# Kernel tuning notes

Hardware: AMD Instinct MI355X
Metric: run time of the kernel (lower is better)

The kernel has to match this reference:

```python
import jax, jax.numpy as jnp
import numpy as np

N, E, F_IN, HID, EF, C = 100000, 1600000, 64, 64, 32, 4

def setup_inputs() -> dict:
    key = jax.random.key(0)
    ks = jax.random.split(key, 24)
    def p(k, shape, scale=0.05):
        return jax.random.normal(k, shape, dtype=jnp.float32) * scale
    return dict(
        x=jax.random.normal(ks[0], (N, F_IN), dtype=jnp.float32),
        edge_index=jax.random.randint(ks[1], (2, E), 0, N, dtype=jnp.int32),
        edge_attr=jax.random.normal(ks[2], (E, EF), dtype=jnp.float32),
        # GCNConv weights for update (z), reset (r), candidate (h) gates
        Wz=p(ks[3], (F_IN, HID)), bz=jnp.zeros((HID,), jnp.float32),
        Wr=p(ks[4], (F_IN, HID)), br=jnp.zeros((HID,), jnp.float32),
        Wh=p(ks[5], (F_IN, HID)), bh=jnp.zeros((HID,), jnp.float32),
        # gate linear layers: Linear(2*HID, HID)
        Wlz=p(ks[6], (2 * HID, HID)), blz=jnp.zeros((HID,), jnp.float32),
        Wlr=p(ks[7], (2 * HID, HID)), blr=jnp.zeros((HID,), jnp.float32),
        Wlh=p(ks[8], (2 * HID, HID)), blh=jnp.zeros((HID,), jnp.float32),
        # edge predictor MLP: Linear(2*HID+EF, HID) -> ReLU -> Dropout(eval) -> Linear(HID, C)
        W1=p(ks[9], (2 * HID + EF, HID)), b1=jnp.zeros((HID,), jnp.float32),
        W2=p(ks[10], (HID, C)), b2=jnp.zeros((C,), jnp.float32),
    )

def _gcn(x, W, b, src, dst, norm, n):
    # GCNConv: out = D^-1/2 (A+I) D^-1/2 (x @ W) + b; src/dst already include self-loops
    xw = x @ W  # [N, HID]
    agg = jax.ops.segment_sum(xw[src] * norm[:, None], dst, num_segments=n)
    return agg + b

def reference(x, edge_index, edge_attr, Wz, bz, Wr, br, Wh, bh,
              Wlz, blz, Wlr, blr, Wlh, blh, W1, b1, W2, b2):
    n = x.shape[0]
    src, dst = edge_index[0], edge_index[1]
    # add self-loops for GCN normalization
    loop = jnp.arange(n, dtype=src.dtype)
    s = jnp.concatenate([src, loop])
    d = jnp.concatenate([dst, loop])
    deg = jax.ops.segment_sum(jnp.ones(s.shape[0], dtype=x.dtype), d, num_segments=n)
    dinv = jax.lax.rsqrt(jnp.maximum(deg, 1.0))
    norm = dinv[s] * dinv[d]  # symmetric normalization per edge
    # TGCN cell, initial hidden state H = zeros
    H0 = jnp.zeros((n, Wz.shape[1]), dtype=x.dtype)
    Z = jax.nn.sigmoid(jnp.concatenate([_gcn(x, Wz, bz, s, d, norm, n), H0], axis=1) @ Wlz + blz)
    R = jax.nn.sigmoid(jnp.concatenate([_gcn(x, Wr, br, s, d, norm, n), H0], axis=1) @ Wlr + blr)
    Ht = jnp.tanh(jnp.concatenate([_gcn(x, Wh, bh, s, d, norm, n), H0 * R], axis=1) @ Wlh + blh)
    h = Z * H0 + (1.0 - Z) * Ht  # [N, HID]
    # edge predictor on original edges (no self-loops)
    emb = jnp.concatenate([h[src], h[dst], edge_attr], axis=1)  # [E, 2*HID+EF]
    hid = jax.nn.relu(emb @ W1 + b1)  # Dropout(0.5) is identity in eval mode
    return hid @ W2 + b2  # [E, C]
```

## Files before the change

kernel.cpp:

```cpp
#include <hip/hip_runtime.h>

#define F 64
#define EF 32
#define COUT 4

typedef unsigned int uint;
typedef unsigned short ushort;
typedef __attribute__((ext_vector_type(8))) short bf16x8;
typedef __attribute__((ext_vector_type(4))) float f32x4;

__device__ inline ushort f2bf(float f) {
    uint u = __float_as_uint(f);
    return (ushort)((u + 0x7fff + ((u >> 16) & 1)) >> 16);
}
__device__ inline float bf2f(ushort u) {
    return __uint_as_float(((uint)u) << 16);
}


__global__ void k_deg(const int* __restrict__ dst, int* __restrict__ deg, int E) {
    int i = blockIdx.x * blockDim.x + threadIdx.x;
    if (i < E) atomicAdd(&deg[dst[i]], 1);
}

__global__ void k_dinv(const int* __restrict__ deg, float* __restrict__ dinv, int n) {
    int i = blockIdx.x * blockDim.x + threadIdx.x;
    if (i < n) dinv[i] = rsqrtf((float)(deg[i] + 1));
}

__global__ void k_xcast(const float* __restrict__ x, ushort* __restrict__ xb, int n4) {
    int i = blockIdx.x * 256 + threadIdx.x;
    if (i >= n4) return;
    float4 v = *(const float4*)(x + (size_t)i * 4);
    ushort4 o;
    o.x = f2bf(v.x); o.y = f2bf(v.y); o.z = f2bf(v.z); o.w = f2bf(v.w);
    *(ushort4*)(xb + (size_t)i * 4) = o;
}


__global__ void k_blocksum(const int* __restrict__ deg, int* __restrict__ bsum, int n) {
    __shared__ int sm[256];
    int i = blockIdx.x * 256 + threadIdx.x;
    sm[threadIdx.x] = (i < n) ? deg[i] : 0;
    __syncthreads();
    for (int s = 128; s > 0; s >>= 1) {
        if (threadIdx.x < s) sm[threadIdx.x] += sm[threadIdx.x + s];
        __syncthreads();
    }
    if (threadIdx.x == 0) bsum[blockIdx.x] = sm[0];
}

__global__ void k_scanb(const int* __restrict__ bsum, int* __restrict__ boffs, int nb) {
    int lane = threadIdx.x;
    int carry = 0;
    for (int base = 0; base < nb; base += 64) {
        int v = (base + lane < nb) ? bsum[base + lane] : 0;
        int incl = v;
        #pragma unroll
        for (int off = 1; off < 64; off <<= 1) {
            int t = __shfl_up(incl, off);
            if (lane >= off) incl += t;
        }
        if (base + lane < nb) boffs[base + lane] = carry + incl - v;
        carry += __shfl(incl, 63);
    }
}

__global__ void k_rowptr(const int* __restrict__ deg, const int* __restrict__ boffs,
                         int* __restrict__ rowptr, int n) {
    __shared__ int sm[256];
    int tid = threadIdx.x;
    int i = blockIdx.x * 256 + tid;
    int v = (i < n) ? deg[i] : 0;
    sm[tid] = v;
    __syncthreads();
    for (int off = 1; off < 256; off <<= 1) {
        int t = (tid >= off) ? sm[tid - off] : 0;
        __syncthreads();
        sm[tid] += t;
        __syncthreads();
    }
    if (i < n) rowptr[i] = boffs[blockIdx.x] + sm[tid] - v;
}

__global__ void k_bucket(const int* __restrict__ src, const int* __restrict__ dst,
                         const int* __restrict__ rowptr, int* __restrict__ fill,
                         int2* __restrict__ es2, int E) {
    int e = blockIdx.x * 256 + threadIdx.x;
    if (e >= E) return;
    int d = dst[e];
    int pos = rowptr[d] + atomicAdd(&fill[d], 1);
    es2[pos] = make_int2(src[e], e);
}

__global__ void k_expand(const int* __restrict__ rowptr, const int* __restrict__ deg,
                         int* __restrict__ edst, int n) {
    int i = blockIdx.x * 256 + threadIdx.x;
    if (i >= n) return;
    int p = rowptr[i], c = deg[i];
    for (int j = 0; j < c; ++j) edst[p + j] = i;
}

__global__ __launch_bounds__(256) void k_agg(
    const ushort* __restrict__ xb, const float* __restrict__ dinv,
    const int2* __restrict__ es2, const int* __restrict__ rowptr,
    const int* __restrict__ deg, ushort* __restrict__ xaggb, int n) {
    int node = (blockIdx.x * 256 + threadIdx.x) >> 6;
    int lane = threadIdx.x & 63;
    if (node >= n) return;
    int start = rowptr[node], cnt = deg[node];
    float di = dinv[node];
    float acc = bf2f(xb[(size_t)node * F + lane]) * di * di;
    for (int base = 0; base < cnt; base += 64) {
        int m = min(64, cnt - base);
        int s = 0; float dv = 0.f;
        if (lane < m) { s = es2[start + base + lane].x; dv = dinv[s]; }
        for (int i = 0; i < m; ++i) {
            int si = __shfl(s, i);
            float wv = __shfl(dv, i) * di;
            acc += bf2f(xb[(size_t)si * F + lane]) * wv;
        }
    }
    xaggb[(size_t)node * F + lane] = f2bf(acc);
}

__global__ void k_weights(const float* __restrict__ Wz, const float* __restrict__ bz,
                          const float* __restrict__ Wh, const float* __restrict__ bh,
                          const float* __restrict__ Wlz, const float* __restrict__ blz,
                          const float* __restrict__ Wlh, const float* __restrict__ blh,
                          ushort* __restrict__ B1t, float* __restrict__ V) {
    int j = threadIdx.x;
    int k = blockIdx.x;
    if (k < 64) {
        float sz = 0.f, sh = 0.f;
        for (int i = 0; i < 64; ++i) {
            sz += Wz[k * 64 + i] * Wlz[i * 64 + j];
            sh += Wh[k * 64 + i] * Wlh[i * 64 + j];
        }
        B1t[j * 64 + k]        = f2bf(sz);
        B1t[(64 + j) * 64 + k] = f2bf(sh);
    } else {
        float sz = blz[j], sh = blh[j];
        for (int i = 0; i < 64; ++i) {
            sz += bz[i] * Wlz[i * 64 + j];
            sh += bh[i] * Wlh[i * 64 + j];
        }
        V[j]      = sz;
        V[64 + j] = sh;
    }
}

__global__ void k_wcast(const float* __restrict__ W1, ushort* __restrict__ B2t,
                        ushort* __restrict__ W1cTb) {
    int i = blockIdx.x * 256 + threadIdx.x;
    if (i < 8192) {
        int c = i >> 6, k = i & 63;
        int row = (c < 64) ? k : (64 + k);
        B2t[i] = f2bf(W1[row * 64 + (c & 63)]);
    }
    int t = i - 8192;
    if (t >= 0 && t < 2048) {
        int j = t >> 5, k = t & 31;
        W1cTb[t] = f2bf(W1[(128 + k) * 64 + j]);
    }
}

__global__ __launch_bounds__(256) void k_node(
    const ushort* __restrict__ xaggb, const ushort* __restrict__ B1t,
    const ushort* __restrict__ B2t, const float* __restrict__ V,
    const float* __restrict__ b1,
    ushort* __restrict__ Pb, ushort* __restrict__ Qb, int n) {
    __shared__ ushort hsm[64 * 64];
    int wid = threadIdx.x >> 6, lane = threadIdx.x & 63;
    int lg = lane >> 4, lc = lane & 15;
    int base = blockIdx.x * 64;

    bf16x8 b1f[2][2], b2f[2][2];
    #pragma unroll
    for (int t = 0; t < 2; ++t) {
        int c1 = ((t ? wid + 4 : wid) * 16 + lc) * 64;
        int c2 = ((wid * 2 + t) * 16 + lc) * 64;
        #pragma unroll
        for (int ks = 0; ks < 2; ++ks) {
            b1f[t][ks] = *(const bf16x8*)(B1t + c1 + ks * 32 + lg * 8);
            b2f[t][ks] = *(const bf16x8*)(B2t + c2 + ks * 32 + lg * 8);
        }
    }
    float vzc = V[wid * 16 + lc], vhc = V[64 + wid * 16 + lc];
    float bP[2];
    #pragma unroll
    for (int t = 0; t < 2; ++t) {
        int c2 = (wid * 2 + t) * 16 + lc;
        bP[t] = (c2 < 64) ? b1[c2] : 0.f;
    }

    const f32x4 fz = {0.f, 0.f, 0.f, 0.f};
    f32x4 accZ[4], accT[4];
    #pragma unroll
    for (int rt = 0; rt < 4; ++rt) { accZ[rt] = fz; accT[rt] = fz; }

    #pragma unroll
    for (int rt = 0; rt < 4; ++rt) {
        const ushort* ap = xaggb + (size_t)(base + rt * 16 + lc) * 64 + lg * 8;
        bf16x8 a0 = *(const bf16x8*)(ap);
        bf16x8 a1 = *(const bf16x8*)(ap + 32);
        accZ[rt] = __builtin_amdgcn_mfma_f32_16x16x32_bf16(a0, b1f[0][0], accZ[rt], 0, 0, 0);
        accZ[rt] = __builtin_amdgcn_mfma_f32_16x16x32_bf16(a1, b1f[0][1], accZ[rt], 0, 0, 0);
        accT[rt] = __builtin_amdgcn_mfma_f32_16x16x32_bf16(a0, b1f[1][0], accT[rt], 0, 0, 0);
        accT[rt] = __builtin_amdgcn_mfma_f32_16x16x32_bf16(a1, b1f[1][1], accT[rt], 0, 0, 0);
    }

    #pragma unroll
    for (int rt = 0; rt < 4; ++rt) {
        #pragma unroll
        for (int r = 0; r < 4; ++r) {
            float z = 1.f / (1.f + __expf(-(accZ[rt][r] + vzc)));
            float tt = tanhf(accT[rt][r] + vhc);
            float h = (1.f - z) * tt;
            int row = rt * 16 + lg * 4 + r;
            int byte = ((row * 64 + wid * 16 + lc) * 2) ^ ((row & 7) << 4);
            *(ushort*)((char*)hsm + byte) = f2bf(h);
        }
    }
    __syncthreads();

    f32x4 acc2[2][4];
    #pragma unroll
    for (int rt = 0; rt < 4; ++rt) { acc2[0][rt] = fz; acc2[1][rt] = fz; }
    #pragma unroll
    for (int rt = 0; rt < 4; ++rt) {
        #pragma unroll
        for (int ks = 0; ks < 2; ++ks) {
            int row = rt * 16 + lc;
            int byte = (row * 128 + ks * 64 + lg * 16) ^ ((row & 7) << 4);
            bf16x8 a2 = *(const bf16x8*)((char*)hsm + byte);
            acc2[0][rt] = __builtin_amdgcn_mfma_f32_16x16x32_bf16(a2, b2f[0][ks], acc2[0][rt], 0, 0, 0);
            acc2[1][rt] = __builtin_amdgcn_mfma_f32_16x16x32_bf16(a2, b2f[1][ks], acc2[1][rt], 0, 0, 0);
        }
    }

    ushort* dstb = (wid < 2) ? Pb : Qb;
    #pragma unroll
    for (int t = 0; t < 2; ++t) {
        int cl = ((wid * 2 + t) * 16 + lc) & 63;
        #pragma unroll
        for (int rt = 0; rt < 4; ++rt) {
            #pragma unroll
            for (int r = 0; r < 4; ++r) {
                int node = base + rt * 16 + lg * 4 + r;
                if (node < n) dstb[(size_t)node * 64 + cl] = f2bf(acc2[t][rt][r] + bP[t]);
            }
        }
    }
}

__global__ __launch_bounds__(256) void k_edge2(
    const int2* __restrict__ es2, const int* __restrict__ edst,
    const float* __restrict__ attr,
    const ushort* __restrict__ Pb, const ushort* __restrict__ Qb,
    const ushort* __restrict__ W1cTb,
    const float* __restrict__ W2, const float* __restrict__ b2,
    float* __restrict__ out, int E) {
    int wid = threadIdx.x >> 6, lane = threadIdx.x & 63;
    int lg = lane >> 4, lc = lane & 15;
    int we = (blockIdx.x * 4 + wid) * 64;
    if (we >= E) return;

    int idx = we + lane; if (idx >= E) idx = E - 1;
    int2 se = es2[idx];
    int sR = se.x, eidR = se.y, dR = edst[idx];

    bf16x8 aW[4];
    #pragma unroll
    for (int rt = 0; rt < 4; ++rt)
        aW[rt] = *(const bf16x8*)(W1cTb + (rt * 16 + lc) * 32 + lg * 8);

    float4 w2r[4][4];
    #pragma unroll
    for (int rt = 0; rt < 4; ++rt)
        #pragma unroll
        for (int r = 0; r < 4; ++r)
            w2r[rt][r] = *(const float4*)(W2 + (rt * 16 + lg * 4 + r) * 4);
    float4 b2v = *(const float4*)(b2);

    const f32x4 fz = {0.f, 0.f, 0.f, 0.f};
    #pragma unroll
    for (int et = 0; et < 4; ++et) {
        int erow = et * 16 + lc;
        int eid_e = __shfl(eidR, erow);
        int s_e   = __shfl(sR, erow);
        int d_e   = __shfl(dR, erow);

        const float* ap = attr + (size_t)eid_e * EF + lg * 8;
        float4 a0 = *(const float4*)(ap);
        float4 a1 = *(const float4*)(ap + 4);
        bf16x8 bfr;
        bfr[0] = (short)f2bf(a0.x); bfr[1] = (short)f2bf(a0.y);
        bfr[2] = (short)f2bf(a0.z); bfr[3] = (short)f2bf(a0.w);
        bfr[4] = (short)f2bf(a1.x); bfr[5] = (short)f2bf(a1.y);
        bfr[6] = (short)f2bf(a1.z); bfr[7] = (short)f2bf(a1.w);

        f32x4 acc[4];
        #pragma unroll
        for (int rt = 0; rt < 4; ++rt) acc[rt] = fz;
        #pragma unroll
        for (int rt = 0; rt < 4; ++rt)
            acc[rt] = __builtin_amdgcn_mfma_f32_16x16x32_bf16(aW[rt], bfr, acc[rt], 0, 0, 0);

        const ushort* Ps = Pb + (size_t)s_e * F;
        const ushort* Qd = Qb + (size_t)d_e * F;
        float o0 = 0.f, o1 = 0.f, o2 = 0.f, o3 = 0.f;
        #pragma unroll
        for (int rt = 0; rt < 4; ++rt) {
            int j0 = rt * 16 + lg * 4;
            uint2 pv = *(const uint2*)(Ps + j0);
            uint2 qv = *(const uint2*)(Qd + j0);
            float p0 = __uint_as_float(pv.x << 16), p1 = __uint_as_float(pv.x & 0xffff0000u);
            float p2 = __uint_as_float(pv.y << 16), p3 = __uint_as_float(pv.y & 0xffff0000u);
            float q0 = __uint_as_float(qv.x << 16), q1 = __uint_as_float(qv.x & 0xffff0000u);
            float q2 = __uint_as_float(qv.y << 16), q3 = __uint_as_float(qv.y & 0xffff0000u);
            float h0 = fmaxf(acc[rt][0] + p0 + q0, 0.f);
            float h1 = fmaxf(acc[rt][1] + p1 + q1, 0.f);
            float h2 = fmaxf(acc[rt][2] + p2 + q2, 0.f);
            float h3 = fmaxf(acc[rt][3] + p3 + q3, 0.f);
            o0 += h0 * w2r[rt][0].x + h1 * w2r[rt][1].x + h2 * w2r[rt][2].x + h3 * w2r[rt][3].x;
            o1 += h0 * w2r[rt][0].y + h1 * w2r[rt][1].y + h2 * w2r[rt][2].y + h3 * w2r[rt][3].y;
            o2 += h0 * w2r[rt][0].z + h1 * w2r[rt][1].z + h2 * w2r[rt][2].z + h3 * w2r[rt][3].z;
            o3 += h0 * w2r[rt][0].w + h1 * w2r[rt][1].w + h2 * w2r[rt][2].w + h3 * w2r[rt][3].w;
        }
        o0 += __shfl_xor(o0, 16); o0 += __shfl_xor(o0, 32);
        o1 += __shfl_xor(o1, 16); o1 += __shfl_xor(o1, 32);
        o2 += __shfl_xor(o2, 16); o2 += __shfl_xor(o2, 32);
        o3 += __shfl_xor(o3, 16); o3 += __shfl_xor(o3, 32);
        if (lg == 0 && (we + erow) < E)
            *(float4*)(out + (size_t)eid_e * 4) =
                make_float4(o0 + b2v.x, o1 + b2v.y, o2 + b2v.z, o3 + b2v.w);
    }
}


extern "C" void kernel_launch(void* const* d_in, const int* in_sizes, int n_in,
                              void* d_out, int out_size, void* d_ws, size_t ws_size,
                              hipStream_t stream) {
    const float* x    = (const float*)d_in[0];
    const int*   ei   = (const int*)d_in[1];
    const float* attr = (const float*)d_in[2];
    const float* Wz   = (const float*)d_in[3];
    const float* bz   = (const float*)d_in[4];
    const float* Wh   = (const float*)d_in[7];
    const float* bh   = (const float*)d_in[8];
    const float* Wlz  = (const float*)d_in[9];
    const float* blz  = (const float*)d_in[10];
    const float* Wlh  = (const float*)d_in[13];
    const float* blh  = (const float*)d_in[14];
    const float* W1   = (const float*)d_in[15];
    const float* b1   = (const float*)d_in[16];
    const float* W2   = (const float*)d_in[17];
    const float* b2   = (const float*)d_in[18];
    float* out = (float*)d_out;

    const int N = in_sizes[0] / F;
    const int E = in_sizes[1] / 2;
    const int* src = ei;
    const int* dst = ei + E;
    const int NB = (N + 255) / 256;
    const int NBT = (N + 63) / 64;

    ushort* xaggb = (ushort*)d_ws;
    ushort* regB  = xaggb + (size_t)N * F;
    ushort* Qb    = regB + (size_t)N * F;
    ushort* B1t   = Qb + (size_t)N * F;
    ushort* B2t   = B1t + 8192;
    ushort* W1cTb = B2t + 8192;
    float*  V     = (float*)(W1cTb + 2048);
    int2*   es2   = (int2*)(V + 128);
    int*    edst  = (int*)(es2 + (size_t)E);
    int*    deg   = edst + E;
    float*  dinv  = (float*)(deg + N);
    int*    rowptr= (int*)(dinv + N);
    int*    fill  = rowptr + N;
    int*    bsum  = fill + N;
    int*    boffs = bsum + 512;
    ushort* xb = regB;
    ushort* Pb = regB;

    hipMemsetAsync(deg, 0, (size_t)N * sizeof(int), stream);
    hipMemsetAsync(fill, 0, (size_t)N * sizeof(int), stream);

    k_deg<<<(E + 255) / 256, 256, 0, stream>>>(dst, deg, E);
    k_dinv<<<NB, 256, 0, stream>>>(deg, dinv, N);
    k_weights<<<65, 64, 0, stream>>>(Wz, bz, Wh, bh, Wlz, blz, Wlh, blh, B1t, V);
    k_wcast<<<40, 256, 0, stream>>>(W1, B2t, W1cTb);
    k_xcast<<<(N * F / 4 + 255) / 256, 256, 0, stream>>>(x, xb, N * F / 4);

    k_blocksum<<<NB, 256, 0, stream>>>(deg, bsum, N);
    k_scanb<<<1, 64, 0, stream>>>(bsum, boffs, NB);
    k_rowptr<<<NB, 256, 0, stream>>>(deg, boffs, rowptr, N);
    k_bucket<<<(E + 255) / 256, 256, 0, stream>>>(src, dst, rowptr, fill, es2, E);
    k_expand<<<NB, 256, 0, stream>>>(rowptr, deg, edst, N);

    k_agg<<<(N * 64 + 255) / 256, 256, 0, stream>>>(xb, dinv, es2, rowptr, deg, xaggb, N);

    k_node<<<NBT, 256, 0, stream>>>(xaggb, B1t, B2t, V, b1, Pb, Qb, N);

    k_edge2<<<(E + 255) / 256, 256, 0, stream>>>(es2, edst, attr, Pb, Qb, W1cTb, W2, b2, out, E);
}
```

Baseline: 430.2 us.

## Process four neighbors per wave in GCN aggregation and stage W2 in LDS

The aggregation kernel changes from one neighbor per iteration across 64 lanes to four neighbors at once. Each 16-lane group loads 4 bf16 features as a uint2 and the groups are combined with xor shuffles. This cuts the serial loop trip count per node by four and widens memory accesses, at the cost of idle lanes on the tail and an extra reduction. The edge kernel also loads W2 and b2 into shared memory instead of keeping 64 float4 registers per thread, which lowers register pressure to improve occupancy but adds a block sync and LDS reads.

```diff
diff --git a/kernel.cpp b/kernel.cpp
--- a/kernel.cpp
+++ b/kernel.cpp
@@ -108,20 +108,41 @@
     int node = (blockIdx.x * 256 + threadIdx.x) >> 6;
     int lane = threadIdx.x & 63;
     if (node >= n) return;
+    int lg = lane >> 4, lc = lane & 15;
     int start = rowptr[node], cnt = deg[node];
     float di = dinv[node];
-    float acc = bf2f(xb[(size_t)node * F + lane]) * di * di;
-    for (int base = 0; base < cnt; base += 64) {
-        int m = min(64, cnt - base);
-        int s = 0; float dv = 0.f;
-        if (lane < m) { s = es2[start + base + lane].x; dv = dinv[s]; }
-        for (int i = 0; i < m; ++i) {
-            int si = __shfl(s, i);
-            float wv = __shfl(dv, i) * di;
-            acc += bf2f(xb[(size_t)si * F + lane]) * wv;
-        }
-    }
-    xaggb[(size_t)node * F + lane] = f2bf(acc);
+    float a0 = 0.f, a1 = 0.f, a2 = 0.f, a3 = 0.f;
+    for (int base = 0; base < cnt; base += 4) {
+        int k = base + lg;
+        float w = 0.f;
+        size_t off = 0;
+        if (k < cnt) {
+            int s = es2[start + k].x;
+            w = dinv[s] * di;
+            off = (size_t)s * F;
+        }
+        uint2 r = make_uint2(0u, 0u);
+        if (k < cnt) r = *(const uint2*)(xb + off + lc * 4);
+        a0 += w * __uint_as_float(r.x << 16);
+        a1 += w * __uint_as_float(r.x & 0xffff0000u);
+        a2 += w * __uint_as_float(r.y << 16);
+        a3 += w * __uint_as_float(r.y & 0xffff0000u);
+    }
+    a0 += __shfl_xor(a0, 16); a0 += __shfl_xor(a0, 32);
+    a1 += __shfl_xor(a1, 16); a1 += __shfl_xor(a1, 32);
+    a2 += __shfl_xor(a2, 16); a2 += __shfl_xor(a2, 32);
+    a3 += __shfl_xor(a3, 16); a3 += __shfl_xor(a3, 32);
+    if (lg == 0) {
+        float dd = di * di;
+        uint2 xv = *(const uint2*)(xb + (size_t)node * F + lc * 4);
+        a0 += dd * __uint_as_float(xv.x << 16);
+        a1 += dd * __uint_as_float(xv.x & 0xffff0000u);
+        a2 += dd * __uint_as_float(xv.y << 16);
+        a3 += dd * __uint_as_float(xv.y & 0xffff0000u);
+        ushort4 o;
+        o.x = f2bf(a0); o.y = f2bf(a1); o.z = f2bf(a2); o.w = f2bf(a3);
+        *(ushort4*)(xaggb + (size_t)node * F + lc * 4) = o;
+    }
 }
 
 __global__ void k_weights(const float* __restrict__ Wz, const float* __restrict__ bz,
@@ -261,6 +282,12 @@
     const ushort* __restrict__ W1cTb,
     const float* __restrict__ W2, const float* __restrict__ b2,
     float* __restrict__ out, int E) {
+    __shared__ float w2s[256];
+    __shared__ float b2s[4];
+    w2s[threadIdx.x] = W2[threadIdx.x];
+    if (threadIdx.x < 4) b2s[threadIdx.x] = b2[threadIdx.x];
+    __syncthreads();
+
     int wid = threadIdx.x >> 6, lane = threadIdx.x & 63;
     int lg = lane >> 4, lc = lane & 15;
     int we = (blockIdx.x * 4 + wid) * 64;
@@ -274,14 +301,6 @@
     #pragma unroll
     for (int rt = 0; rt < 4; ++rt)
         aW[rt] = *(const bf16x8*)(W1cTb + (rt * 16 + lc) * 32 + lg * 8);
-
-    float4 w2r[4][4];
-    #pragma unroll
-    for (int rt = 0; rt < 4; ++rt)
-        #pragma unroll
-        for (int r = 0; r < 4; ++r)
-            w2r[rt][r] = *(const float4*)(W2 + (rt * 16 + lg * 4 + r) * 4);
-    float4 b2v = *(const float4*)(b2);
 
     const f32x4 fz = {0.f, 0.f, 0.f, 0.f};
     #pragma unroll
@@ -323,10 +342,14 @@
             float h1 = fmaxf(acc[rt][1] + p1 + q1, 0.f);
             float h2 = fmaxf(acc[rt][2] + p2 + q2, 0.f);
             float h3 = fmaxf(acc[rt][3] + p3 + q3, 0.f);
-            o0 += h0 * w2r[rt][0].x + h1 * w2r[rt][1].x + h2 * w2r[rt][2].x + h3 * w2r[rt][3].x;
-            o1 += h0 * w2r[rt][0].y + h1 * w2r[rt][1].y + h2 * w2r[rt][2].y + h3 * w2r[rt][3].y;
-            o2 += h0 * w2r[rt][0].z + h1 * w2r[rt][1].z + h2 * w2r[rt][2].z + h3 * w2r[rt][3].z;
-            o3 += h0 * w2r[rt][0].w + h1 * w2r[rt][1].w + h2 * w2r[rt][2].w + h3 * w2r[rt][3].w;
+            float4 w0 = *(const float4*)(&w2s[(j0 + 0) * 4]);
+            float4 w1 = *(const float4*)(&w2s[(j0 + 1) * 4]);
+            float4 w2v = *(const float4*)(&w2s[(j0 + 2) * 4]);
+            float4 w3 = *(const float4*)(&w2s[(j0 + 3) * 4]);
+            o0 += h0 * w0.x + h1 * w1.x + h2 * w2v.x + h3 * w3.x;
+            o1 += h0 * w0.y + h1 * w1.y + h2 * w2v.y + h3 * w3.y;
+            o2 += h0 * w0.z + h1 * w1.z + h2 * w2v.z + h3 * w3.z;
+            o3 += h0 * w0.w + h1 * w1.w + h2 * w2v.w + h3 * w3.w;
         }
         o0 += __shfl_xor(o0, 16); o0 += __shfl_xor(o0, 32);
         o1 += __shfl_xor(o1, 16); o1 += __shfl_xor(o1, 32);
@@ -334,7 +357,7 @@
         o3 += __shfl_xor(o3, 16); o3 += __shfl_xor(o3, 32);
         if (lg == 0 && (we + erow) < E)
             *(float4*)(out + (size_t)eid_e * 4) =
-                make_float4(o0 + b2v.x, o1 + b2v.y, o2 + b2v.z, o3 + b2v.w);
+                make_float4(o0 + b2s[0], o1 + b2s[1], o2 + b2s[2], o3 + b2s[3]);
     }
 }
 
```

Result: faster. 416.8 us (-3.1%).
